# Kernel tuning notes

Hardware: AMD Instinct MI355X
Metric: run time of the kernel (lower is better)

Reference implementation:

```python
import jax, jax.numpy as jnp
import numpy as np

B, S, DM = 4, 2048, 1024
H, D = 16, 64  # nb_head, size_per_head
NEG = 1e12


def setup_inputs() -> dict:
    key = jax.random.key(0)
    ks = jax.random.split(key, 8)
    return {
        "Q_seq": jax.random.normal(ks[0], (B, S, DM), dtype=jnp.float32),
        "K_seq": jax.random.normal(ks[1], (B, S, DM), dtype=jnp.float32),
        "V_seq": jax.random.normal(ks[2], (B, S, DM), dtype=jnp.float32),
        "Q_len": jax.random.randint(ks[3], (B, 1), 0, S, dtype=jnp.int32),
        "V_len": jax.random.randint(ks[4], (B, 1), 0, S, dtype=jnp.int32),
        "WQ": jax.random.normal(ks[5], (DM, H * D), dtype=jnp.float32) * 0.02,
        "WK": jax.random.normal(ks[6], (DM, H * D), dtype=jnp.float32) * 0.02,
        "WV": jax.random.normal(ks[7], (DM, H * D), dtype=jnp.float32) * 0.02,
    }


def reference(Q_seq, K_seq, V_seq, Q_len, V_len, WQ, WK, WV):
    b, sq, _ = Q_seq.shape
    sk = K_seq.shape[1]
    # project and split heads -> [B, H, S, D]
    q = (Q_seq @ WQ).reshape(b, sq, H, D).transpose(0, 2, 1, 3)
    k = (K_seq @ WK).reshape(b, sk, H, D).transpose(0, 2, 1, 3)
    v = (V_seq @ WV).reshape(b, sk, H, D).transpose(0, 2, 1, 3)
    # scores [B, H, Sq, Sk]
    A = jnp.einsum("bhqd,bhkd->bhqk", q, k) / jnp.sqrt(jnp.float32(D))
    # key-length mask: positions t < V_len are valid (1 - cumsum(one_hot))
    kmask = (jnp.arange(sk)[None, :] < V_len[:, 0:1]).astype(A.dtype)  # [B, Sk]
    A = A - (1.0 - kmask)[:, None, None, :] * NEG
    A = jax.nn.softmax(A, axis=-1)
    O = jnp.einsum("bhqk,bhkd->bhqd", A, v)
    O = O.transpose(0, 2, 1, 3).reshape(b, sq, H * D)
    # query-length mask (multiplicative)
    qmask = (jnp.arange(sq)[None, :] < Q_len[:, 0:1]).astype(O.dtype)  # [B, Sq]
    return O * qmask[:, :, None]
```

## Files before the change

### kernel.cpp

```cpp
#include <hip/hip_runtime.h>
#include <hip/hip_bf16.h>
#include <math.h>

#define BATCH 4
#define SEQ   2048
#define DM    1024
#define NHEAD 16
#define HDIM  64
#define MROWS (BATCH*SEQ)

typedef float f32x4 __attribute__((ext_vector_type(4)));
typedef float f32x16 __attribute__((ext_vector_type(16)));
typedef short bf16x8 __attribute__((ext_vector_type(8)));
typedef unsigned int u32x4 __attribute__((ext_vector_type(4)));

typedef __attribute__((address_space(1))) unsigned int as1_u32;
typedef __attribute__((address_space(3))) unsigned int as3_u32;

__device__ __forceinline__ void gld16(const void* g, void* l) {
    __builtin_amdgcn_global_load_lds((const as1_u32*)g, (as3_u32*)l, 16, 0, 0);
}

__device__ __forceinline__ unsigned short f2bf(float f) {
    unsigned int u = __float_as_uint(f);
    u += 0x7FFFu + ((u >> 16) & 1u);
    return (unsigned short)(u >> 16);
}

__device__ __forceinline__ unsigned int pack2bf(float a, float b) {
    return (unsigned int)f2bf(a) | ((unsigned int)f2bf(b) << 16);
}

__device__ __forceinline__ float fexp2(float x) {
    float r;
    asm("v_exp_f32 %0, %1" : "=v"(r) : "v"(x));
    return r;
}

__device__ __forceinline__ unsigned int cvtpk2(float lo, float hi) {
    unsigned int r;
    asm("v_cvt_pk_bf16_f32 %0, %1, %2" : "=v"(r) : "v"(lo), "v"(hi));
    return r;
}

__device__ __forceinline__ int row_limit(int len, int lmode) {
    if (lmode == 0) return (len + 31) & ~31;
    if (lmode == 1) return (len <= 0) ? 0 : ((len + 63) & ~63);
    return (len <= 0) ? SEQ : ((len + 63) & ~63);
}

__global__ __launch_bounds__(256) void convx3_kernel(const float* __restrict__ Q,
                                                     const float* __restrict__ K,
                                                     const float* __restrict__ V,
                                                     unsigned short* __restrict__ Xq,
                                                     unsigned short* __restrict__ Xk,
                                                     unsigned short* __restrict__ Xv,
                                                     const int* __restrict__ Qlen,
                                                     const int* __restrict__ Vlen,
                                                     int zoff) {
    const int z = blockIdx.y + zoff;
    const float* in = (z == 0) ? Q : (z == 1) ? K : V;
    unsigned short* out = (z == 0) ? Xq : (z == 1) ? Xk : Xv;
    int i = blockIdx.x * 256 + threadIdx.x;
    int row = i >> 7;
    int b = row >> 11, s = row & 2047;
    int lim = (z == 0) ? row_limit(Qlen[b], 0) : row_limit(Vlen[b], z);
    if (s >= lim) return;
    const float4* p = reinterpret_cast<const float4*>(in) + (size_t)i * 2;
    float4 a = p[0], v = p[1];
    uint4 r;
    r.x = pack2bf(a.x, a.y);
    r.y = pack2bf(a.z, a.w);
    r.z = pack2bf(v.x, v.y);
    r.w = pack2bf(v.z, v.w);
    reinterpret_cast<uint4*>(out)[i] = r;
}

__global__ __launch_bounds__(256) void convw3_kernel(const float* __restrict__ WQ,
                                                     const float* __restrict__ WK,
                                                     const float* __restrict__ WV,
                                                     unsigned short* __restrict__ Oq,
                                                     unsigned short* __restrict__ Ok,
                                                     unsigned short* __restrict__ Ov,
                                                     int zoff) {
    const int z = blockIdx.z + zoff;
    const float* in = (z == 0) ? WQ : (z == 1) ? WK : WV;
    unsigned short* out = (z == 0) ? Oq : (z == 1) ? Ok : Ov;
    const float scale = (z == 0) ? 0.125f * 1.44269504088896340736f : 1.0f;
    __shared__ float tile[64][65];
    int n0 = blockIdx.x * 64, k0 = blockIdx.y * 64;
    int tx = threadIdx.x, ty = threadIdx.y;
#pragma unroll
    for (int i = 0; i < 64; i += 4)
        tile[ty + i][tx] = in[(size_t)(k0 + ty + i) * DM + n0 + tx];
    __syncthreads();
#pragma unroll
    for (int i = 0; i < 64; i += 4)
        out[(size_t)(n0 + ty + i) * DM + k0 + tx] = f2bf(tile[tx][ty + i] * scale);
}

__global__ __launch_bounds__(256) void gemm3_kernel(const unsigned short* __restrict__ Xq,
                                                    const unsigned short* __restrict__ Xk,
                                                    const unsigned short* __restrict__ Xv,
                                                    const unsigned short* __restrict__ Wq,
                                                    const unsigned short* __restrict__ Wk,
                                                    const unsigned short* __restrict__ Wv,
                                                    unsigned short* __restrict__ qo,
                                                    unsigned short* __restrict__ ko,
                                                    unsigned short* __restrict__ vo,
                                                    const int* __restrict__ Qlen,
                                                    const int* __restrict__ Vlen,
                                                    int zoff) {
    const int z = blockIdx.z + zoff;
    const unsigned short* A = (z == 0) ? Xq : (z == 1) ? Xk : Xv;
    const unsigned short* Bt = (z == 0) ? Wq : (z == 1) ? Wk : Wv;
    unsigned short* out = (z == 0) ? qo : (z == 1) ? ko : vo;
    const int vmode = (z == 2);
    const int m0 = blockIdx.y << 7, n0 = blockIdx.x << 7;
    {
        int b = m0 >> 11, s0 = m0 & 2047;
        int len = (z == 0) ? Qlen[b] : Vlen[b];
        if (s0 >= row_limit(len, z)) return;
    }
    __shared__ unsigned short lA[128 * 32];
    __shared__ unsigned short lB[128 * 32];
    const int tid = threadIdx.x, lane = tid & 63, wave = tid >> 6;
    const int wr = wave >> 1, wc = wave & 1;
    const int col = lane & 15, grp = lane >> 4;

    f32x4 acc[4][4] = {};

    const int srow = tid >> 2, sseg = tid & 3;
    const unsigned short* srcA0 = A + (size_t)(m0 + srow) * DM + sseg * 8;
    const unsigned short* srcA1 = srcA0 + (size_t)64 * DM;
    const unsigned short* srcB0 = Bt + (size_t)(n0 + srow) * DM + sseg * 8;
    const unsigned short* srcB1 = srcB0 + (size_t)64 * DM;
    unsigned short* dA0 = &lA[wave * 512];
    unsigned short* dA1 = &lA[2048 + wave * 512];
    unsigned short* dB0 = &lB[wave * 512];
    unsigned short* dB1 = &lB[2048 + wave * 512];

    for (int k0 = 0; k0 < DM; k0 += 32) {
        __syncthreads();
        gld16(srcA0 + k0, dA0);
        gld16(srcA1 + k0, dA1);
        gld16(srcB0 + k0, dB0);
        gld16(srcB1 + k0, dB1);
        __syncthreads();

        bf16x8 af[4], bfr[4];
#pragma unroll
        for (int mt = 0; mt < 4; mt++)
            af[mt] = *reinterpret_cast<const bf16x8*>(&lA[(wr * 64 + mt * 16 + col) * 32 + grp * 8]);
#pragma unroll
        for (int nt = 0; nt < 4; nt++)
            bfr[nt] = *reinterpret_cast<const bf16x8*>(&lB[(wc * 64 + nt * 16 + col) * 32 + grp * 8]);
#pragma unroll
        for (int mt = 0; mt < 4; mt++)
#pragma unroll
            for (int nt = 0; nt < 4; nt++)
                acc[mt][nt] = __builtin_amdgcn_mfma_f32_16x16x32_bf16(af[mt], bfr[nt], acc[mt][nt], 0, 0, 0);
    }

#pragma unroll
    for (int mt = 0; mt < 4; mt++) {
        int rowb = m0 + wr * 64 + mt * 16 + grp * 4;
#pragma unroll
        for (int nt = 0; nt < 4; nt++) {
            int c = n0 + wc * 64 + nt * 16 + col;
            int h = c >> 6, d = c & 63;
            if (vmode == 0) {
#pragma unroll
                for (int r = 0; r < 4; r++) {
                    int rr = rowb + r;
                    int b = rr >> 11, s = rr & 2047;
                    out[((((size_t)(b * NHEAD + h)) << 11) + s) * HDIM + d] = f2bf(acc[mt][nt][r]);
                }
            } else {
                int b = rowb >> 11, s = rowb & 2047;
                uint2 pk;
                pk.x = pack2bf(acc[mt][nt][0], acc[mt][nt][1]);
                pk.y = pack2bf(acc[mt][nt][2], acc[mt][nt][3]);
                *reinterpret_cast<uint2*>(
                    &out[(((size_t)(b * NHEAD + h)) * HDIM + d) * SEQ + s]) = pk;
            }
        }
    }
}

__global__ __launch_bounds__(256) void flash_kernel(const unsigned short* __restrict__ qm,
                                                    const unsigned short* __restrict__ km,
                                                    const unsigned short* __restrict__ vtm,
                                                    const int* __restrict__ Qlen,
                                                    const int* __restrict__ Vlen,
                                                    float* __restrict__ out) {
    const int raw = blockIdx.x;
    const int x = raw & 7, y = raw >> 3;
    const int qt = y & 15, z = y >> 4;
    const int h = x + ((z & 1) << 3);
    const int b = z >> 1;
    const int q0 = qt << 7;
    const int lane = threadIdx.x & 63, wv = threadIdx.x >> 6;
    const int qI = lane & 31, hi = lane >> 5;
    const int ql = Qlen[b], vl = Vlen[b];
    const int qrow = q0 + wv * 32 + qI;

    if (q0 >= ql) {
        int r = threadIdx.x >> 1;
        int c0 = (threadIdx.x & 1) * 32;
        float* p = out + (size_t)(b * SEQ + q0 + r) * DM + h * HDIM + c0;
        float4 z4 = {0.f, 0.f, 0.f, 0.f};
#pragma unroll
        for (int i = 0; i < 8; i++) reinterpret_cast<float4*>(p)[i] = z4;
        return;
    }

    const bool uniform = (vl <= 0);
    const int eff = uniform ? SEQ : vl;
    const int nkv = (eff + 63) >> 6;

    const size_t hb = ((size_t)(b * NHEAD + h)) << 11;
    const unsigned short* qbase = qm + hb * HDIM;
    const unsigned short* kbase = km + hb * HDIM;
    const unsigned short* vbase = vtm + hb * HDIM;

    __shared__ __align__(16) unsigned short lsK[2][64 * 64];
    __shared__ __align__(16) unsigned short lsV[2][64 * 64];

    const int r8 = lane >> 3, cs = lane & 7;
    const int sx = cs ^ r8;
    const size_t offK0 = (size_t)(wv * 16 + r8) * HDIM + sx * 8;
    const size_t offK1 = offK0 + (size_t)8 * HDIM;
    const size_t offV0 = (size_t)(wv * 16 + r8) * SEQ + sx * 8;
    const size_t offV1 = offV0 + (size_t)8 * SEQ;

#define STAGE(BF, KV0) do {                                              \
        const unsigned short* gk_ = kbase + (size_t)(KV0) * HDIM;        \
        const unsigned short* gv_ = vbase + (KV0);                       \
        gld16(gk_ + offK0, &lsK[BF][(wv * 16) * 64]);                    \
        gld16(gk_ + offK1, &lsK[BF][(wv * 16 + 8) * 64]);                \
        gld16(gv_ + offV0, &lsV[BF][(wv * 16) * 64]);                    \
        gld16(gv_ + offV1, &lsV[BF][(wv * 16 + 8) * 64]);                \
    } while (0)

    bf16x8 qB[4];
#pragma unroll
    for (int sp = 0; sp < 4; sp++)
        qB[sp] = *reinterpret_cast<const bf16x8*>(&qbase[(size_t)qrow * HDIM + sp * 16 + hi * 8]);

    f32x16 o_acc2[2] = {};
    float m = -3.0e38f, l = 0.f;
    const int q7 = qI & 7;

    STAGE(0, 0);
    __syncthreads();

    int bf = 0;
    for (int kv = 0; kv < nkv; kv++) {
        const int kv0 = kv << 6;
        if (kv + 1 < nkv) STAGE(bf ^ 1, (kv + 1) << 6);

        f32x16 st2[2] = {};
        const unsigned short* Kb = &lsK[bf][0];
        __builtin_amdgcn_s_setprio(1);
#pragma unroll
        for (int kt = 0; kt < 2; kt++)
#pragma unroll
            for (int sp = 0; sp < 4; sp++) {
                int xs = (sp * 2 + hi) ^ q7;
                bf16x8 ka = *reinterpret_cast<const bf16x8*>(&Kb[(kt * 32 + qI) * 64 + xs * 8]);
                st2[kt] = __builtin_amdgcn_mfma_f32_32x32x16_bf16(ka, qB[sp], st2[kt], 0, 0, 0);
            }
        __builtin_amdgcn_s_setprio(0);

        if (uniform) {
#pragma unroll
            for (int t = 0; t < 2; t++)
#pragma unroll
                for (int r = 0; r < 16; r++) st2[t][r] = 0.f;
        } else if (kv0 + 64 > eff) {
#pragma unroll
            for (int t = 0; t < 2; t++)
#pragma unroll
                for (int r = 0; r < 16; r++)
                    if (kv0 + t * 32 + (r & 3) + 8 * (r >> 2) + 4 * hi >= eff)
                        st2[t][r] = -1e30f;
        }

        float tm8[8], ts8[8];
#pragma unroll
        for (int r = 0; r < 8; r++)
            tm8[r] = fmaxf(fmaxf(st2[0][r], st2[0][r + 8]), fmaxf(st2[1][r], st2[1][r + 8]));
        float tm4[4];
#pragma unroll
        for (int r = 0; r < 4; r++) tm4[r] = fmaxf(tm8[r], tm8[r + 4]);
        float mx = fmaxf(fmaxf(tm4[0], tm4[1]), fmaxf(tm4[2], tm4[3]));
        mx = fmaxf(mx, __shfl_xor(mx, 32));
        float mnew = fmaxf(m, mx);
        float sc = fexp2(m - mnew);
#pragma unroll
        for (int t = 0; t < 2; t++)
#pragma unroll
            for (int r = 0; r < 16; r++) st2[t][r] = fexp2(st2[t][r] - mnew);
#pragma unroll
        for (int r = 0; r < 8; r++)
            ts8[r] = (st2[0][r] + st2[0][r + 8]) + (st2[1][r] + st2[1][r + 8]);
        float ts4[4];
#pragma unroll
        for (int r = 0; r < 4; r++) ts4[r] = ts8[r] + ts8[r + 4];
        float rs = (ts4[0] + ts4[1]) + (ts4[2] + ts4[3]);
        rs += __shfl_xor(rs, 32);
        l = l * sc + rs;
        m = mnew;
        o_acc2[0] *= sc;
        o_acc2[1] *= sc;

        unsigned int pk[2][8];
#pragma unroll
        for (int t = 0; t < 2; t++)
#pragma unroll
            for (int p = 0; p < 8; p++)
                pk[t][p] = cvtpk2(st2[t][2 * p], st2[t][2 * p + 1]);

        const unsigned short* Vb = &lsV[bf][0];
#pragma unroll
        for (int ks = 0; ks < 4; ks++) {
            const int t = ks >> 1, c = (ks & 1) * 4;
            unsigned int sel0 = pk[t][c], sel1 = pk[t][c + 1];
            unsigned int sel2 = pk[t][c + 2], sel3 = pk[t][c + 3];
            unsigned int sendA = hi ? sel0 : sel2;
            unsigned int sendB = hi ? sel1 : sel3;
            unsigned int gotA = __shfl_xor(sendA, 32);
            unsigned int gotB = __shfl_xor(sendB, 32);
            u32x4 u;
            u[0] = hi ? gotA : sel0;
            u[1] = hi ? gotB : sel1;
            u[2] = hi ? sel2 : gotA;
            u[3] = hi ? sel3 : gotB;
            bf16x8 pB = __builtin_bit_cast(bf16x8, u);
            int xs = (ks * 2 + hi) ^ q7;
            __builtin_amdgcn_s_setprio(1);
#pragma unroll
            for (int dt = 0; dt < 2; dt++) {
                bf16x8 va = *reinterpret_cast<const bf16x8*>(&Vb[(dt * 32 + qI) * 64 + xs * 8]);
                o_acc2[dt] = __builtin_amdgcn_mfma_f32_32x32x16_bf16(va, pB, o_acc2[dt], 0, 0, 0);
            }
            __builtin_amdgcn_s_setprio(0);
        }

        __syncthreads();
        bf ^= 1;
    }
#undef STAGE

    const float rl = 1.0f / l;
    const bool live = (qrow < ql);
    float* obase = out + (size_t)(b * SEQ + qrow) * DM + h * HDIM;
#pragma unroll
    for (int dt = 0; dt < 2; dt++)
#pragma unroll
        for (int a = 0; a < 4; a++) {
            float4 val;
            val.x = live ? o_acc2[dt][4 * a + 0] * rl : 0.f;
            val.y = live ? o_acc2[dt][4 * a + 1] * rl : 0.f;
            val.z = live ? o_acc2[dt][4 * a + 2] * rl : 0.f;
            val.w = live ? o_acc2[dt][4 * a + 3] * rl : 0.f;
            *reinterpret_cast<float4*>(&obase[dt * 32 + a * 8 + hi * 4]) = val;
        }
}

extern "C" void kernel_launch(void* const* d_in, const int* in_sizes, int n_in,
                              void* d_out, int out_size, void* d_ws, size_t ws_size,
                              hipStream_t stream) {
    const float* Q_seq = (const float*)d_in[0];
    const float* K_seq = (const float*)d_in[1];
    const float* V_seq = (const float*)d_in[2];
    const int* Q_len = (const int*)d_in[3];
    const int* V_len = (const int*)d_in[4];
    const float* WQ = (const float*)d_in[5];
    const float* WK = (const float*)d_in[6];
    const float* WV = (const float*)d_in[7];
    float* out = (float*)d_out;

    const size_t XN = (size_t)MROWS * DM;
    const size_t WN = (size_t)DM * DM;
    const size_t need_fast = (6 * XN + 3 * WN) * sizeof(unsigned short);

    const int cx_grid = MROWS * DM / 8 / 256;
    dim3 cw_grid(DM / 64, DM / 64, 3), cw_blk(64, 4);
    dim3 g_grid(DM / 128, MROWS / 128, 3), g_blk(256);

    if (ws_size >= need_fast) {
        unsigned short* Xq = (unsigned short*)d_ws;
        unsigned short* Xk = Xq + XN;
        unsigned short* Xv = Xk + XN;
        unsigned short* Wq = Xv + XN;
        unsigned short* Wk = Wq + WN;
        unsigned short* Wv = Wk + WN;
        unsigned short* qb = Wv + WN;
        unsigned short* kb = qb + XN;
        unsigned short* vtb = kb + XN;

        convx3_kernel<<<dim3(cx_grid, 3), 256, 0, stream>>>(Q_seq, K_seq, V_seq,
                                                            Xq, Xk, Xv, Q_len, V_len, 0);
        convw3_kernel<<<cw_grid, cw_blk, 0, stream>>>(WQ, WK, WV, Wq, Wk, Wv, 0);
        gemm3_kernel<<<g_grid, g_blk, 0, stream>>>(Xq, Xk, Xv, Wq, Wk, Wv,
                                                   qb, kb, vtb, Q_len, V_len, 0);
        flash_kernel<<<dim3(1024), 256, 0, stream>>>(qb, kb, vtb, Q_len, V_len, out);
    } else {
        unsigned short* Xbuf = (unsigned short*)d_ws;
        unsigned short* Wt = Xbuf + XN;
        unsigned short* qb = Wt + WN;
        unsigned short* kb = qb + XN;
        unsigned short* vtb = kb + XN;
        dim3 cw1(DM / 64, DM / 64, 1);
        dim3 g1(DM / 128, MROWS / 128, 1);
        for (int z = 0; z < 3; z++) {
            convx3_kernel<<<dim3(cx_grid, 1), 256, 0, stream>>>(Q_seq, K_seq, V_seq,
                                                                Xbuf, Xbuf, Xbuf, Q_len, V_len, z);
            convw3_kernel<<<cw1, cw_blk, 0, stream>>>(WQ, WK, WV, Wt, Wt, Wt, z);
            gemm3_kernel<<<g1, g_blk, 0, stream>>>(Xbuf, Xbuf, Xbuf, Wt, Wt, Wt,
                                                   qb, kb, vtb, Q_len, V_len, z);
        }
        flash_kernel<<<dim3(1024), 256, 0, stream>>>(qb, kb, vtb, Q_len, V_len, out);
    }
}
```

Measured before the change: 144.5 us.

## Split KV loop across two wave groups in flash kernel and merge partial softmax

Doubles the flash block to 512 threads: four query waves are each paired with two KV-split waves, which process alternating 64-key tiles with their own double-buffered LDS. At the end, the two halves exchange m/l and half of the output accumulator through LDS, then merge them with the usual log-sum-exp rescaling, each wave writing 32 of the 64 head dims. The aim is to halve the serial KV-loop length per block and add more waves per CU to hide latency. In exchange it adds a final LDS reduction and a second sync, doubles LDS use, and drops the setprio hints.

```diff
diff --git a/kernel.cpp b/kernel.cpp
--- a/kernel.cpp
+++ b/kernel.cpp
@@ -188,7 +188,7 @@
     }
 }
 
-__global__ __launch_bounds__(256) void flash_kernel(const unsigned short* __restrict__ qm,
+__global__ __launch_bounds__(512) void flash_kernel(const unsigned short* __restrict__ qm,
                                                     const unsigned short* __restrict__ km,
                                                     const unsigned short* __restrict__ vtm,
                                                     const int* __restrict__ Qlen,
@@ -201,17 +201,20 @@
     const int b = z >> 1;
     const int q0 = qt << 7;
     const int lane = threadIdx.x & 63, wv = threadIdx.x >> 6;
+    const int qw = wv & 3, kw = wv >> 2;
     const int qI = lane & 31, hi = lane >> 5;
     const int ql = Qlen[b], vl = Vlen[b];
-    const int qrow = q0 + wv * 32 + qI;
+    const int qrow = q0 + qw * 32 + qI;
 
     if (q0 >= ql) {
-        int r = threadIdx.x >> 1;
-        int c0 = (threadIdx.x & 1) * 32;
+        int r = threadIdx.x >> 2;
+        int c0 = (threadIdx.x & 3) * 16;
         float* p = out + (size_t)(b * SEQ + q0 + r) * DM + h * HDIM + c0;
         float4 z4 = {0.f, 0.f, 0.f, 0.f};
-#pragma unroll
-        for (int i = 0; i < 8; i++) reinterpret_cast<float4*>(p)[i] = z4;
+        reinterpret_cast<float4*>(p)[0] = z4;
+        reinterpret_cast<float4*>(p)[1] = z4;
+        reinterpret_cast<float4*>(p)[2] = z4;
+        reinterpret_cast<float4*>(p)[3] = z4;
         return;
     }
 
@@ -224,23 +227,24 @@
     const unsigned short* kbase = km + hb * HDIM;
     const unsigned short* vbase = vtm + hb * HDIM;
 
-    __shared__ __align__(16) unsigned short lsK[2][64 * 64];
-    __shared__ __align__(16) unsigned short lsV[2][64 * 64];
+    __shared__ __align__(16) unsigned short lsK[2][2][64 * 64];
+    __shared__ __align__(16) unsigned short lsV[2][2][64 * 64];
 
     const int r8 = lane >> 3, cs = lane & 7;
     const int sx = cs ^ r8;
-    const size_t offK0 = (size_t)(wv * 16 + r8) * HDIM + sx * 8;
+    const size_t offK0 = (size_t)(qw * 16 + r8) * HDIM + sx * 8;
     const size_t offK1 = offK0 + (size_t)8 * HDIM;
-    const size_t offV0 = (size_t)(wv * 16 + r8) * SEQ + sx * 8;
+    const size_t offV0 = (size_t)(qw * 16 + r8) * SEQ + sx * 8;
     const size_t offV1 = offV0 + (size_t)8 * SEQ;
 
-#define STAGE(BF, KV0) do {                                              \
-        const unsigned short* gk_ = kbase + (size_t)(KV0) * HDIM;        \
-        const unsigned short* gv_ = vbase + (KV0);                       \
-        gld16(gk_ + offK0, &lsK[BF][(wv * 16) * 64]);                    \
-        gld16(gk_ + offK1, &lsK[BF][(wv * 16 + 8) * 64]);                \
-        gld16(gv_ + offV0, &lsV[BF][(wv * 16) * 64]);                    \
-        gld16(gv_ + offV1, &lsV[BF][(wv * 16 + 8) * 64]);                \
+#define STAGE(BF, T) do {                                                \
+        const int kv0_ = (T) << 6;                                       \
+        const unsigned short* gk_ = kbase + (size_t)kv0_ * HDIM;         \
+        const unsigned short* gv_ = vbase + kv0_;                        \
+        gld16(gk_ + offK0, &lsK[kw][BF][(qw * 16) * 64]);                \
+        gld16(gk_ + offK1, &lsK[kw][BF][(qw * 16 + 8) * 64]);            \
+        gld16(gv_ + offV0, &lsV[kw][BF][(qw * 16) * 64]);                \
+        gld16(gv_ + offV1, &lsV[kw][BF][(qw * 16 + 8) * 64]);            \
     } while (0)
 
     bf16x8 qB[4];
@@ -252,100 +256,103 @@
     float m = -3.0e38f, l = 0.f;
     const int q7 = qI & 7;
 
-    STAGE(0, 0);
+    const int rounds = (nkv + 1) >> 1;
+    if (kw < nkv) STAGE(0, kw);
     __syncthreads();
 
     int bf = 0;
-    for (int kv = 0; kv < nkv; kv++) {
-        const int kv0 = kv << 6;
-        if (kv + 1 < nkv) STAGE(bf ^ 1, (kv + 1) << 6);
-
-        f32x16 st2[2] = {};
-        const unsigned short* Kb = &lsK[bf][0];
-        __builtin_amdgcn_s_setprio(1);
-#pragma unroll
-        for (int kt = 0; kt < 2; kt++)
-#pragma unroll
-            for (int sp = 0; sp < 4; sp++) {
-                int xs = (sp * 2 + hi) ^ q7;
-                bf16x8 ka = *reinterpret_cast<const bf16x8*>(&Kb[(kt * 32 + qI) * 64 + xs * 8]);
-                st2[kt] = __builtin_amdgcn_mfma_f32_32x32x16_bf16(ka, qB[sp], st2[kt], 0, 0, 0);
+    for (int r = 0; r < rounds; r++) {
+        const int tcur = 2 * r + kw;
+        const int tnext = tcur + 2;
+        if (tnext < nkv) STAGE(bf ^ 1, tnext);
+
+        if (tcur < nkv) {
+            const int kv0 = tcur << 6;
+
+            f32x16 st2[2] = {};
+            const unsigned short* Kb = &lsK[kw][bf][0];
+#pragma unroll
+            for (int kt = 0; kt < 2; kt++)
+#pragma unroll
+                for (int sp = 0; sp < 4; sp++) {
+                    int xs = (sp * 2 + hi) ^ q7;
+                    bf16x8 ka = *reinterpret_cast<const bf16x8*>(&Kb[(kt * 32 + qI) * 64 + xs * 8]);
+                    st2[kt] = __builtin_amdgcn_mfma_f32_32x32x16_bf16(ka, qB[sp], st2[kt], 0, 0, 0);
+                }
+
+            if (uniform) {
+#pragma unroll
+                for (int t = 0; t < 2; t++)
+#pragma unroll
+                    for (int rr = 0; rr < 16; rr++) st2[t][rr] = 0.f;
+            } else if (kv0 + 64 > eff) {
+#pragma unroll
+                for (int t = 0; t < 2; t++)
+#pragma unroll
+                    for (int rr = 0; rr < 16; rr++)
+                        if (kv0 + t * 32 + (rr & 3) + 8 * (rr >> 2) + 4 * hi >= eff)
+                            st2[t][rr] = -1e30f;
             }
-        __builtin_amdgcn_s_setprio(0);
-
-        if (uniform) {
+
+            float tm8[8];
+#pragma unroll
+            for (int rr = 0; rr < 8; rr++)
+                tm8[rr] = fmaxf(fmaxf(st2[0][rr], st2[0][rr + 8]), fmaxf(st2[1][rr], st2[1][rr + 8]));
+            float tm4[4];
+#pragma unroll
+            for (int rr = 0; rr < 4; rr++) tm4[rr] = fmaxf(tm8[rr], tm8[rr + 4]);
+            float mx = fmaxf(fmaxf(tm4[0], tm4[1]), fmaxf(tm4[2], tm4[3]));
+            mx = fmaxf(mx, __shfl_xor(mx, 32));
+            float mnew = fmaxf(m, mx);
+            float sc = fexp2(m - mnew);
 #pragma unroll
             for (int t = 0; t < 2; t++)
 #pragma unroll
-                for (int r = 0; r < 16; r++) st2[t][r] = 0.f;
-        } else if (kv0 + 64 > eff) {
+                for (int rr = 0; rr < 16; rr++) st2[t][rr] = fexp2(st2[t][rr] - mnew);
+            float ts8[8];
+#pragma unroll
+            for (int rr = 0; rr < 8; rr++)
+                ts8[rr] = (st2[0][rr] + st2[0][rr + 8]) + (st2[1][rr] + st2[1][rr + 8]);
+            float ts4[4];
+#pragma unroll
+            for (int rr = 0; rr < 4; rr++) ts4[rr] = ts8[rr] + ts8[rr + 4];
+            float rs = (ts4[0] + ts4[1]) + (ts4[2] + ts4[3]);
+            rs += __shfl_xor(rs, 32);
+            l = l * sc + rs;
+            m = mnew;
+            o_acc2[0] *= sc;
+            o_acc2[1] *= sc;
+
+            unsigned int pk[2][8];
 #pragma unroll
             for (int t = 0; t < 2; t++)
 #pragma unroll
-                for (int r = 0; r < 16; r++)
-                    if (kv0 + t * 32 + (r & 3) + 8 * (r >> 2) + 4 * hi >= eff)
-                        st2[t][r] = -1e30f;
-        }
-
-        float tm8[8], ts8[8];
-#pragma unroll
-        for (int r = 0; r < 8; r++)
-            tm8[r] = fmaxf(fmaxf(st2[0][r], st2[0][r + 8]), fmaxf(st2[1][r], st2[1][r + 8]));
-        float tm4[4];
-#pragma unroll
-        for (int r = 0; r < 4; r++) tm4[r] = fmaxf(tm8[r], tm8[r + 4]);
-        float mx = fmaxf(fmaxf(tm4[0], tm4[1]), fmaxf(tm4[2], tm4[3]));
-        mx = fmaxf(mx, __shfl_xor(mx, 32));
-        float mnew = fmaxf(m, mx);
-        float sc = fexp2(m - mnew);
-#pragma unroll
-        for (int t = 0; t < 2; t++)
-#pragma unroll
-            for (int r = 0; r < 16; r++) st2[t][r] = fexp2(st2[t][r] - mnew);
-#pragma unroll
-        for (int r = 0; r < 8; r++)
-            ts8[r] = (st2[0][r] + st2[0][r + 8]) + (st2[1][r] + st2[1][r + 8]);
-        float ts4[4];
-#pragma unroll
-        for (int r = 0; r < 4; r++) ts4[r] = ts8[r] + ts8[r + 4];
-        float rs = (ts4[0] + ts4[1]) + (ts4[2] + ts4[3]);
-        rs += __shfl_xor(rs, 32);
-        l = l * sc + rs;
-        m = mnew;
-        o_acc2[0] *= sc;
-        o_acc2[1] *= sc;
-
-        unsigned int pk[2][8];
-#pragma unroll
-        for (int t = 0; t < 2; t++)
-#pragma unroll
-            for (int p = 0; p < 8; p++)
-                pk[t][p] = cvtpk2(st2[t][2 * p], st2[t][2 * p + 1]);
-
-        const unsigned short* Vb = &lsV[bf][0];
-#pragma unroll
-        for (int ks = 0; ks < 4; ks++) {
-            const int t = ks >> 1, c = (ks & 1) * 4;
-            unsigned int sel0 = pk[t][c], sel1 = pk[t][c + 1];
-            unsigned int sel2 = pk[t][c + 2], sel3 = pk[t][c + 3];
-            unsigned int sendA = hi ? sel0 : sel2;
-            unsigned int sendB = hi ? sel1 : sel3;
-            unsigned int gotA = __shfl_xor(sendA, 32);
-            unsigned int gotB = __shfl_xor(sendB, 32);
-            u32x4 u;
-            u[0] = hi ? gotA : sel0;
-            u[1] = hi ? gotB : sel1;
-            u[2] = hi ? sel2 : gotA;
-            u[3] = hi ? sel3 : gotB;
-            bf16x8 pB = __builtin_bit_cast(bf16x8, u);
-            int xs = (ks * 2 + hi) ^ q7;
-            __builtin_amdgcn_s_setprio(1);
-#pragma unroll
-            for (int dt = 0; dt < 2; dt++) {
-                bf16x8 va = *reinterpret_cast<const bf16x8*>(&Vb[(dt * 32 + qI) * 64 + xs * 8]);
-                o_acc2[dt] = __builtin_amdgcn_mfma_f32_32x32x16_bf16(va, pB, o_acc2[dt], 0, 0, 0);
+                for (int p = 0; p < 8; p++)
+                    pk[t][p] = cvtpk2(st2[t][2 * p], st2[t][2 * p + 1]);
+
+            const unsigned short* Vb = &lsV[kw][bf][0];
+#pragma unroll
+            for (int ks = 0; ks < 4; ks++) {
+                const int t = ks >> 1, c = (ks & 1) * 4;
+                unsigned int sel0 = pk[t][c], sel1 = pk[t][c + 1];
+                unsigned int sel2 = pk[t][c + 2], sel3 = pk[t][c + 3];
+                unsigned int sendA = hi ? sel0 : sel2;
+                unsigned int sendB = hi ? sel1 : sel3;
+                unsigned int gotA = __shfl_xor(sendA, 32);
+                unsigned int gotB = __shfl_xor(sendB, 32);
+                u32x4 u;
+                u[0] = hi ? gotA : sel0;
+                u[1] = hi ? gotB : sel1;
+                u[2] = hi ? sel2 : gotA;
+                u[3] = hi ? sel3 : gotB;
+                bf16x8 pB = __builtin_bit_cast(bf16x8, u);
+                int xs = (ks * 2 + hi) ^ q7;
+#pragma unroll
+                for (int dt = 0; dt < 2; dt++) {
+                    bf16x8 va = *reinterpret_cast<const bf16x8*>(&Vb[(dt * 32 + qI) * 64 + xs * 8]);
+                    o_acc2[dt] = __builtin_amdgcn_mfma_f32_32x32x16_bf16(va, pB, o_acc2[dt], 0, 0, 0);
+                }
             }
-            __builtin_amdgcn_s_setprio(0);
         }
 
         __syncthreads();
@@ -353,20 +360,36 @@
     }
 #undef STAGE
 
-    const float rl = 1.0f / l;
+    float* osc = (float*)&lsK[0][0][0];
+    float* mls = (float*)&lsV[0][0][0];
+    const int self = (wv << 6) + lane;
+    const int peer = ((wv ^ 4) << 6) + lane;
+    f32x16 o_keep = (kw == 0) ? o_acc2[0] : o_acc2[1];
+    f32x16 o_give = (kw == 0) ? o_acc2[1] : o_acc2[0];
+    mls[self * 2] = m;
+    mls[self * 2 + 1] = l;
+#pragma unroll
+    for (int i = 0; i < 16; i++) osc[self * 16 + i] = o_give[i];
+    __syncthreads();
+    const float m2 = mls[peer * 2], l2 = mls[peer * 2 + 1];
+    const float msh = fmaxf(m, m2);
+    const float f1 = fexp2(m - msh), f2 = fexp2(m2 - msh);
+    const float rl = 1.0f / (f1 * l + f2 * l2);
     const bool live = (qrow < ql);
     float* obase = out + (size_t)(b * SEQ + qrow) * DM + h * HDIM;
 #pragma unroll
-    for (int dt = 0; dt < 2; dt++)
-#pragma unroll
-        for (int a = 0; a < 4; a++) {
-            float4 val;
-            val.x = live ? o_acc2[dt][4 * a + 0] * rl : 0.f;
-            val.y = live ? o_acc2[dt][4 * a + 1] * rl : 0.f;
-            val.z = live ? o_acc2[dt][4 * a + 2] * rl : 0.f;
-            val.w = live ? o_acc2[dt][4 * a + 3] * rl : 0.f;
-            *reinterpret_cast<float4*>(&obase[dt * 32 + a * 8 + hi * 4]) = val;
-        }
+    for (int a = 0; a < 4; a++) {
+        float4 val;
+        float v0 = f1 * o_keep[4 * a + 0] + f2 * osc[peer * 16 + 4 * a + 0];
+        float v1 = f1 * o_keep[4 * a + 1] + f2 * osc[peer * 16 + 4 * a + 1];
+        float v2 = f1 * o_keep[4 * a + 2] + f2 * osc[peer * 16 + 4 * a + 2];
+        float v3 = f1 * o_keep[4 * a + 3] + f2 * osc[peer * 16 + 4 * a + 3];
+        val.x = live ? v0 * rl : 0.f;
+        val.y = live ? v1 * rl : 0.f;
+        val.z = live ? v2 * rl : 0.f;
+        val.w = live ? v3 * rl : 0.f;
+        *reinterpret_cast<float4*>(&obase[kw * 32 + a * 8 + hi * 4]) = val;
+    }
 }
 
 extern "C" void kernel_launch(void* const* d_in, const int* in_sizes, int n_in,
@@ -406,7 +429,7 @@
         convw3_kernel<<<cw_grid, cw_blk, 0, stream>>>(WQ, WK, WV, Wq, Wk, Wv, 0);
         gemm3_kernel<<<g_grid, g_blk, 0, stream>>>(Xq, Xk, Xv, Wq, Wk, Wv,
                                                    qb, kb, vtb, Q_len, V_len, 0);
-        flash_kernel<<<dim3(1024), 256, 0, stream>>>(qb, kb, vtb, Q_len, V_len, out);
+        flash_kernel<<<dim3(1024), 512, 0, stream>>>(qb, kb, vtb, Q_len, V_len, out);
     } else {
         unsigned short* Xbuf = (unsigned short*)d_ws;
         unsigned short* Wt = Xbuf + XN;
@@ -422,6 +445,6 @@
             gemm3_kernel<<<g1, g_blk, 0, stream>>>(Xbuf, Xbuf, Xbuf, Wt, Wt, Wt,
                                                    qb, kb, vtb, Q_len, V_len, z);
         }
-        flash_kernel<<<dim3(1024), 256, 0, stream>>>(qb, kb, vtb, Q_len, V_len, out);
-    }
-}
+        flash_kernel<<<dim3(1024), 512, 0, stream>>>(qb, kb, vtb, Q_len, V_len, out);
+    }
+}
```

After: 133.6 us. 1.08x faster.
